# Kernel tuning notes

Measured on AMD Instinct MI355X. Metric: run time of the kernel, lower is better.

The kernel has to match this reference:

```python
import jax, jax.numpy as jnp
import numpy as np

B, T, N, D = 8, 64, 128, 128  # batch, timesteps, num_nodes, hidden_dim
LN_EPS = 1e-5
L2_EPS = 1e-12


def setup_inputs() -> dict:
    key = jax.random.key(0)
    ks = jax.random.split(key, 8)
    feat = jax.random.normal(ks[0], (B, T, N, D), dtype=jnp.float32)
    w = jax.random.uniform(ks[1], (D,), dtype=jnp.float32)  # learned adj gate (torch.rand init)
    s = 1.0 / np.sqrt(D)
    W1 = jax.random.uniform(ks[2], (D, D), dtype=jnp.float32, minval=-s, maxval=s)
    b1 = jax.random.uniform(ks[3], (D,), dtype=jnp.float32, minval=-s, maxval=s)
    W2 = jax.random.uniform(ks[4], (D, D), dtype=jnp.float32, minval=-s, maxval=s)
    b2 = jax.random.uniform(ks[5], (D,), dtype=jnp.float32, minval=-s, maxval=s)
    gamma = jnp.ones((D,), dtype=jnp.float32)
    beta = jnp.zeros((D,), dtype=jnp.float32)
    return {"feat": feat, "w": w, "W1": W1, "b1": b1, "W2": W2, "b2": b2,
            "gamma": gamma, "beta": beta}


def _windows(x):
    # x: (B, T, N, D) -> (B, T-2, 3*N, D): 3 consecutive timesteps flattened over nodes
    b, t, n, d = x.shape
    return jnp.stack([x[:, i:i + t - 2] for i in range(3)], axis=2).reshape(b, t - 2, 3 * n, d)


def reference(feat, w, W1, b1, W2, b2, gamma, beta):
    # gated + L2-normalized features for learned adjacency
    wf = feat * jax.nn.sigmoid(w)
    wf = wf / jnp.maximum(jnp.linalg.norm(wf, axis=-1, keepdims=True), L2_EPS)

    win = _windows(feat)   # (B, T-2, 3N, D)
    wwin = _windows(wf)    # (B, T-2, 3N, D)

    # learned adjacency: gram matrix per window, (B, T-2, 3N, 3N)
    adj = jnp.einsum('btmd,btnd->btmn', wwin, wwin)

    # symmetric normalization D^{-1/2} A D^{-1/2}; inf/nan (deg<=0) -> 0 as in torch
    deg = adj.sum(axis=-1, keepdims=True)
    dis = jnp.where(deg > 0, jax.lax.rsqrt(jnp.maximum(deg, 1e-38)), 0.0)
    nadj = dis * adj * jnp.swapaxes(dis, -1, -2)

    # message passing, keep last N rows (current timestep)
    agg = jnp.einsum('btmn,btnd->btmd', nadj, win)[:, :, -N:, :]

    # FFN (dropout is identity in eval): Linear -> ReLU -> Linear
    h = jax.nn.relu(agg @ W1 + b1) @ W2 + b2

    # residual with current-timestep features + LayerNorm
    s = feat[:, 2:] + h
    mu = s.mean(axis=-1, keepdims=True)
    var = ((s - mu) ** 2).mean(axis=-1, keepdims=True)
    return (s - mu) * jax.lax.rsqrt(var + LN_EPS) * gamma + beta
```

## Files before the change

### kernel.cpp

```cpp
#include <hip/hip_runtime.h>
#include <math.h>

#define BB    8
#define TDIM  64
#define NN    128
#define DD    128
#define TTOUT 62
#define W3    384

typedef __attribute__((ext_vector_type(8))) short bf16x8;
typedef __attribute__((ext_vector_type(4))) float f32x4;

__device__ __forceinline__ float sigf(float x){ return 1.0f/(1.0f+__expf(-x)); }
__device__ __forceinline__ unsigned short f2bf(float x){
  union{float f; unsigned u;} v; v.f=x;
  unsigned r = v.u + 0x7FFFu + ((v.u>>16)&1u);
  return (unsigned short)(r>>16);
}
__device__ __forceinline__ int swzA(int row, int col){ return row*128 + (col ^ ((row&7)<<3)); }
__device__ __forceinline__ int swzF(int row, int col){ return row*64  + (col ^ ((row&7)<<3)); }

__global__ __launch_bounds__(512) void k_pre(const float* __restrict__ feat,
    const float* __restrict__ w, const float* __restrict__ W1, const float* __restrict__ W2,
    float* __restrict__ rscale, float* __restrict__ ssum,
    unsigned short* __restrict__ W1T, unsigned short* __restrict__ W2T){
  __shared__ float sSig[DD];
  __shared__ float sRs[NN];
  __shared__ float sPart[4*DD];
  const int bid = blockIdx.x, tid = threadIdx.x;
  if(bid >= BB*TDIM){
    const float* W = (bid == BB*TDIM) ? W1 : W2;
    unsigned short* WT = (bid == BB*TDIM) ? W1T : W2T;
    for(int e=tid; e<DD*DD; e+=512){
      int k = e>>7, n = e&127;
      WT[n*DD + k] = f2bf(W[(size_t)k*DD + n]);
    }
    return;
  }
  const int bt = bid;
  if(tid < DD) sSig[tid] = sigf(w[tid]);
  __syncthreads();
  const int row = tid >> 2, q = tid & 3;
  const float* fp = feat + ((size_t)bt*NN + row)*DD + q*32;
  float ss = 0.f;
  #pragma unroll
  for(int i=0;i<8;i++){
    float4 v = *(const float4*)(fp + i*4);
    float g0 = v.x*sSig[q*32+i*4+0], g1 = v.y*sSig[q*32+i*4+1];
    float g2 = v.z*sSig[q*32+i*4+2], g3 = v.w*sSig[q*32+i*4+3];
    ss += g0*g0 + g1*g1 + g2*g2 + g3*g3;
  }
  ss += __shfl_xor(ss,1); ss += __shfl_xor(ss,2);
  float rs = 1.0f / fmaxf(sqrtf(ss), 1e-12f);
  if(q==0){ rscale[(size_t)bt*NN + row] = rs; sRs[row] = rs; }
  __syncthreads();
  const int d = tid & 127, rg = tid >> 7;
  const float* fc = feat + ((size_t)bt*NN + rg*32)*DD + d;
  float acc = 0.f;
  #pragma unroll 8
  for(int i=0;i<32;i++) acc += fc[(size_t)i*DD] * sRs[rg*32+i];
  sPart[rg*DD + d] = acc;
  __syncthreads();
  if(tid < DD)
    ssum[(size_t)bt*DD + tid] =
      (sPart[tid] + sPart[DD+tid] + sPart[2*DD+tid] + sPart[3*DD+tid]) * sSig[tid];
}

__global__ void k_dis(const float* __restrict__ feat, const float* __restrict__ w,
                      const float* __restrict__ rscale, const float* __restrict__ ssum,
                      float* __restrict__ dis){
  __shared__ float s3[DD];
  __shared__ float sg[DD];
  int bt2 = (blockIdx.x & 7)*62 + (blockIdx.x >> 3);
  int b = bt2 / TTOUT, tt = bt2 % TTOUT;
  int tid = threadIdx.x;
  if(tid < DD){
    int base = (b*TDIM + tt)*DD;
    s3[tid] = ssum[base+tid] + ssum[base+DD+tid] + ssum[base+2*DD+tid];
    sg[tid] = sigf(w[tid]);
  }
  __syncthreads();
  int gr = (b*TDIM + tt)*NN + tid;
  const float4* fr = (const float4*)(feat + (size_t)gr*DD);
  float deg = 0.f;
  #pragma unroll 8
  for(int q=0;q<DD/4;q++){
    float4 f = fr[q];
    deg += f.x*sg[q*4+0]*s3[q*4+0] + f.y*sg[q*4+1]*s3[q*4+1]
         + f.z*sg[q*4+2]*s3[q*4+2] + f.w*sg[q*4+3]*s3[q*4+3];
  }
  deg *= rscale[gr];
  dis[(size_t)bt2*W3 + tid] = (deg > 0.f) ? rsqrtf(fmaxf(deg, 1e-38f)) : 0.f;
}

__global__ __launch_bounds__(512,4) void k_main(
    const float* __restrict__ feat,
    const float* __restrict__ w,
    const float* __restrict__ rscale, const float* __restrict__ dis,
    const unsigned short* __restrict__ W1T, const float* __restrict__ b1,
    const unsigned short* __restrict__ W2T, const float* __restrict__ b2,
    const float* __restrict__ gamma, const float* __restrict__ beta,
    float* __restrict__ out)
{
  __shared__ __align__(16) unsigned short sm[36864];
  __shared__ float sSig[DD];
  unsigned short* sA  = sm;
  unsigned short* sG  = sm + 16384;
  unsigned short* sFt = sm + 20480;
  unsigned short* sP  = sm + 28672;
  unsigned short* sWt = sm + 16384;

  const int tid = threadIdx.x;
  const int bid = blockIdx.x;
  const int bt2 = (bid & 7)*62 + (bid >> 3);
  const int rowBase = (bt2/TTOUT)*TDIM*NN + (bt2%TTOUT)*NN;
  const float* disP = dis + (size_t)bt2*W3;

  const int lane = tid & 63, wid = tid >> 6;
  const int l15 = lane & 15, l4 = lane >> 4;
  const int m0 = wid * 16;

  if(tid < DD) sSig[tid] = sigf(w[tid]);
  __syncthreads();

  #pragma unroll
  for(int e0=0; e0<8; ++e0){
    int e = e0*512 + tid;
    int d = e & 127, r0 = (e>>7)*4;
    float sg = sSig[d];
    #pragma unroll
    for(int i=0;i<4;i++){
      int j = 256 + r0 + i, gr = rowBase + j;
      float f = feat[(size_t)gr*DD + d];
      float fac = rscale[gr]*disP[j];
      sA[swzA(r0+i, d)] = f2bf(f*sg*fac);
    }
  }

  f32x4 acc2[8];
  #pragma unroll
  for(int i=0;i<8;i++) acc2[i] = (f32x4){0.f,0.f,0.f,0.f};

  for(int c=0; c<12; ++c){
    const int n0 = c*32;
    __syncthreads();
    #pragma unroll
    for(int e0=0; e0<2; ++e0){
      int e = e0*512 + tid;
      int d = e & 127, r0 = (e>>7)*4;
      float sg = sSig[d];
      unsigned short fb[4];
      #pragma unroll
      for(int i=0;i<4;i++){
        int j = n0 + r0 + i, gr = rowBase + j;
        float f = feat[(size_t)gr*DD + d];
        float fac = rscale[gr]*disP[j];
        fb[i] = f2bf(f);
        sG[swzA(r0+i, d)] = f2bf(f*sg*fac);
      }
      unsigned int* fp = (unsigned int*)&sFt[swzF(d, r0)];
      fp[0] = (unsigned)fb[0] | ((unsigned)fb[1]<<16);
      fp[1] = (unsigned)fb[2] | ((unsigned)fb[3]<<16);
    }
    __syncthreads();

    f32x4 p0 = {0.f,0.f,0.f,0.f}, p1 = {0.f,0.f,0.f,0.f};
    #pragma unroll
    for(int ks=0; ks<4; ++ks){
      bf16x8 aA  = *(const bf16x8*)&sA[swzA(m0+l15, ks*32 + l4*8)];
      bf16x8 bg0 = *(const bf16x8*)&sG[swzA( 0+l15, ks*32 + l4*8)];
      bf16x8 bg1 = *(const bf16x8*)&sG[swzA(16+l15, ks*32 + l4*8)];
      p0 = __builtin_amdgcn_mfma_f32_16x16x32_bf16(aA, bg0, p0, 0,0,0);
      p1 = __builtin_amdgcn_mfma_f32_16x16x32_bf16(aA, bg1, p1, 0,0,0);
    }
    #pragma unroll
    for(int r=0;r<4;r++){
      sP[swzF(m0 + l4*4 + r,  0 + l15)] = f2bf(p0[r]);
      sP[swzF(m0 + l4*4 + r, 16 + l15)] = f2bf(p1[r]);
    }
    __syncthreads();

    bf16x8 aP = *(const bf16x8*)&sP[swzF(m0+l15, l4*8)];
    #pragma unroll
    for(int dt=0; dt<8; ++dt){
      bf16x8 bF = *(const bf16x8*)&sFt[swzF(dt*16+l15, l4*8)];
      acc2[dt] = __builtin_amdgcn_mfma_f32_16x16x32_bf16(aP, bF, acc2[dt], 0,0,0);
    }
  }

  unsigned short* ovl = sA;
  #pragma unroll
  for(int dt=0; dt<8; ++dt)
    #pragma unroll
    for(int r=0;r<4;r++)
      ovl[swzA(m0+l4*4+r, dt*16+l15)] = f2bf(acc2[dt][r]);

  f32x4 acch[8];
  #pragma unroll
  for(int dt=0; dt<8; ++dt){
    float bv = b1[dt*16+l15];
    acch[dt] = (f32x4){bv,bv,bv,bv};
  }
  for(int kh=0; kh<2; ++kh){
    __syncthreads();
    #pragma unroll
    for(int it=0; it<2; ++it){
      int e = it*512 + tid, n = e>>3, sg2 = e&7;
      uint4 v = *(const uint4*)(W1T + (size_t)n*DD + kh*64 + sg2*8);
      *(uint4*)&sWt[swzF(n, sg2*8)] = v;
    }
    __syncthreads();
    #pragma unroll
    for(int ks=0; ks<2; ++ks){
      bf16x8 aA = *(const bf16x8*)&ovl[swzA(m0+l15, kh*64 + ks*32 + l4*8)];
      #pragma unroll
      for(int dt=0; dt<8; ++dt){
        bf16x8 bW = *(const bf16x8*)&sWt[swzF(dt*16+l15, ks*32 + l4*8)];
        acch[dt] = __builtin_amdgcn_mfma_f32_16x16x32_bf16(aA, bW, acch[dt], 0,0,0);
      }
    }
  }
  __syncthreads();
  #pragma unroll
  for(int dt=0; dt<8; ++dt)
    #pragma unroll
    for(int r=0;r<4;r++)
      ovl[swzA(m0+l4*4+r, dt*16+l15)] = f2bf(fmaxf(acch[dt][r], 0.f));

  f32x4 acco[8];
  #pragma unroll
  for(int dt=0; dt<8; ++dt){
    float bv = b2[dt*16+l15];
    acco[dt] = (f32x4){bv,bv,bv,bv};
  }
  for(int kh=0; kh<2; ++kh){
    __syncthreads();
    #pragma unroll
    for(int it=0; it<2; ++it){
      int e = it*512 + tid, n = e>>3, sg2 = e&7;
      uint4 v = *(const uint4*)(W2T + (size_t)n*DD + kh*64 + sg2*8);
      *(uint4*)&sWt[swzF(n, sg2*8)] = v;
    }
    __syncthreads();
    #pragma unroll
    for(int ks=0; ks<2; ++ks){
      bf16x8 aA = *(const bf16x8*)&ovl[swzA(m0+l15, kh*64 + ks*32 + l4*8)];
      #pragma unroll
      for(int dt=0; dt<8; ++dt){
        bf16x8 bW = *(const bf16x8*)&sWt[swzF(dt*16+l15, ks*32 + l4*8)];
        acco[dt] = __builtin_amdgcn_mfma_f32_16x16x32_bf16(aA, bW, acco[dt], 0,0,0);
      }
    }
  }

  const float* fres = feat + (size_t)(rowBase + 256)*DD;
  #pragma unroll
  for(int r=0;r<4;r++){
    int m = m0 + l4*4 + r;
    float vals[8]; float s1 = 0.f, s2 = 0.f;
    #pragma unroll
    for(int dt=0; dt<8; ++dt){
      int d = dt*16 + l15;
      float v = acco[dt][r] + fres[(size_t)m*DD + d];
      vals[dt] = v; s1 += v; s2 += v*v;
    }
    #pragma unroll
    for(int k=1;k<16;k<<=1){ s1 += __shfl_xor(s1,k); s2 += __shfl_xor(s2,k); }
    float mu   = s1*(1.0f/DD);
    float rstd = rsqrtf(s2*(1.0f/DD) - mu*mu + 1e-5f);
    #pragma unroll
    for(int dt=0; dt<8; ++dt){
      int d = dt*16 + l15;
      out[((size_t)bt2*NN + m)*DD + d] = (vals[dt]-mu)*rstd*gamma[d] + beta[d];
    }
  }
}

extern "C" void kernel_launch(void* const* d_in, const int* in_sizes, int n_in,
                              void* d_out, int out_size, void* d_ws, size_t ws_size,
                              hipStream_t stream){
  const float* feat  = (const float*)d_in[0];
  const float* w     = (const float*)d_in[1];
  const float* W1    = (const float*)d_in[2];
  const float* b1    = (const float*)d_in[3];
  const float* W2    = (const float*)d_in[4];
  const float* b2    = (const float*)d_in[5];
  const float* gamma = (const float*)d_in[6];
  const float* beta  = (const float*)d_in[7];
  float* out = (float*)d_out;

  char* ws = (char*)d_ws;
  float* rscale = (float*)(ws + 0);
  float* ssum   = (float*)(ws + 262144);
  float* dis    = (float*)(ws + 524288);
  unsigned short* W1T = (unsigned short*)(ws + 1286144);
  unsigned short* W2T = (unsigned short*)(ws + 1318912);

  k_pre<<<BB*TDIM + 2, 512, 0, stream>>>(feat, w, W1, W2, rscale, ssum, W1T, W2T);
  k_dis<<<BB*TTOUT, W3, 0, stream>>>(feat, w, rscale, ssum, dis);
  k_main<<<BB*TTOUT, 512, 0, stream>>>(feat, w, rscale, dis, W1T, b1, W2T, b2,
                                       gamma, beta, out);
}
```

Baseline: 98.63 us.

## Keep A operand in registers, pad LDS layouts, shrink shared memory for occupancy

The current-timestep A-tile is now loaded directly from global memory into per-wave bf16 registers instead of being staged in LDS. The XOR swizzles are replaced with padded row strides, and the LDS buffers are re-aliased, cutting the shared footprint from about 72KB to about 52KB. Launch bounds go from 4 to 6 blocks per CU so that more blocks can be resident. The trade-off is extra register pressure under the tighter bound, possible spills, and padded layouts that may show different bank-conflict behaviour than the swizzle.

Result: slower. 152.6 us (+54.7%).

```diff
diff --git a/kernel.cpp b/kernel.cpp
--- a/kernel.cpp
+++ b/kernel.cpp
@@ -7,6 +7,9 @@
 #define DD    128
 #define TTOUT 62
 #define W3    384
+#define LG    136
+#define LP    40
+#define LW    68
 
 typedef __attribute__((ext_vector_type(8))) short bf16x8;
 typedef __attribute__((ext_vector_type(4))) float f32x4;
@@ -17,8 +20,6 @@
   unsigned r = v.u + 0x7FFFu + ((v.u>>16)&1u);
   return (unsigned short)(r>>16);
 }
-__device__ __forceinline__ int swzA(int row, int col){ return row*128 + (col ^ ((row&7)<<3)); }
-__device__ __forceinline__ int swzF(int row, int col){ return row*64  + (col ^ ((row&7)<<3)); }
 
 __global__ __launch_bounds__(512) void k_pre(const float* __restrict__ feat,
     const float* __restrict__ w, const float* __restrict__ W1, const float* __restrict__ W2,
@@ -93,7 +94,7 @@
   dis[(size_t)bt2*W3 + tid] = (deg > 0.f) ? rsqrtf(fmaxf(deg, 1e-38f)) : 0.f;
 }
 
-__global__ __launch_bounds__(512,4) void k_main(
+__global__ __launch_bounds__(512,6) void k_main(
     const float* __restrict__ feat,
     const float* __restrict__ w,
     const float* __restrict__ rscale, const float* __restrict__ dis,
@@ -102,13 +103,13 @@
     const float* __restrict__ gamma, const float* __restrict__ beta,
     float* __restrict__ out)
 {
-  __shared__ __align__(16) unsigned short sm[36864];
+  __shared__ __align__(16) unsigned short sm[26112];
   __shared__ float sSig[DD];
-  unsigned short* sA  = sm;
-  unsigned short* sG  = sm + 16384;
-  unsigned short* sFt = sm + 20480;
-  unsigned short* sP  = sm + 28672;
-  unsigned short* sWt = sm + 16384;
+  unsigned short* sG  = sm;
+  unsigned short* sFt = sm + 4352;
+  unsigned short* sP  = sm + 9472;
+  unsigned short* ovl = sm;
+  unsigned short* sWt = sm + 17408;
 
   const int tid = threadIdx.x;
   const int bid = blockIdx.x;
@@ -123,17 +124,22 @@
   if(tid < DD) sSig[tid] = sigf(w[tid]);
   __syncthreads();
 
-  #pragma unroll
-  for(int e0=0; e0<8; ++e0){
-    int e = e0*512 + tid;
-    int d = e & 127, r0 = (e>>7)*4;
-    float sg = sSig[d];
-    #pragma unroll
-    for(int i=0;i<4;i++){
-      int j = 256 + r0 + i, gr = rowBase + j;
-      float f = feat[(size_t)gr*DD + d];
-      float fac = rscale[gr]*disP[j];
-      sA[swzA(r0+i, d)] = f2bf(f*sg*fac);
+  bf16x8 aReg[4];
+  {
+    const int j = 256 + m0 + l15, gr = rowBase + j;
+    const float fac = rscale[gr]*disP[j];
+    const float* fr = feat + (size_t)gr*DD;
+    #pragma unroll
+    for(int ks=0; ks<4; ++ks){
+      float4 v0 = *(const float4*)(fr + ks*32 + l4*8);
+      float4 v1 = *(const float4*)(fr + ks*32 + l4*8 + 4);
+      const float* sg = sSig + ks*32 + l4*8;
+      unsigned short o[8];
+      o[0]=f2bf(v0.x*sg[0]*fac); o[1]=f2bf(v0.y*sg[1]*fac);
+      o[2]=f2bf(v0.z*sg[2]*fac); o[3]=f2bf(v0.w*sg[3]*fac);
+      o[4]=f2bf(v1.x*sg[4]*fac); o[5]=f2bf(v1.y*sg[5]*fac);
+      o[6]=f2bf(v1.z*sg[6]*fac); o[7]=f2bf(v1.w*sg[7]*fac);
+      aReg[ks] = *(bf16x8*)o;
     }
   }
 
@@ -156,9 +162,9 @@
         float f = feat[(size_t)gr*DD + d];
         float fac = rscale[gr]*disP[j];
         fb[i] = f2bf(f);
-        sG[swzA(r0+i, d)] = f2bf(f*sg*fac);
+        sG[(r0+i)*LG + d] = f2bf(f*sg*fac);
       }
-      unsigned int* fp = (unsigned int*)&sFt[swzF(d, r0)];
+      unsigned int* fp = (unsigned int*)&sFt[d*LP + r0];
       fp[0] = (unsigned)fb[0] | ((unsigned)fb[1]<<16);
       fp[1] = (unsigned)fb[2] | ((unsigned)fb[3]<<16);
     }
@@ -167,33 +173,33 @@
     f32x4 p0 = {0.f,0.f,0.f,0.f}, p1 = {0.f,0.f,0.f,0.f};
     #pragma unroll
     for(int ks=0; ks<4; ++ks){
-      bf16x8 aA  = *(const bf16x8*)&sA[swzA(m0+l15, ks*32 + l4*8)];
-      bf16x8 bg0 = *(const bf16x8*)&sG[swzA( 0+l15, ks*32 + l4*8)];
-      bf16x8 bg1 = *(const bf16x8*)&sG[swzA(16+l15, ks*32 + l4*8)];
-      p0 = __builtin_amdgcn_mfma_f32_16x16x32_bf16(aA, bg0, p0, 0,0,0);
-      p1 = __builtin_amdgcn_mfma_f32_16x16x32_bf16(aA, bg1, p1, 0,0,0);
+      bf16x8 bg0 = *(const bf16x8*)&sG[( 0+l15)*LG + ks*32 + l4*8];
+      bf16x8 bg1 = *(const bf16x8*)&sG[(16+l15)*LG + ks*32 + l4*8];
+      p0 = __builtin_amdgcn_mfma_f32_16x16x32_bf16(aReg[ks], bg0, p0, 0,0,0);
+      p1 = __builtin_amdgcn_mfma_f32_16x16x32_bf16(aReg[ks], bg1, p1, 0,0,0);
     }
     #pragma unroll
     for(int r=0;r<4;r++){
-      sP[swzF(m0 + l4*4 + r,  0 + l15)] = f2bf(p0[r]);
-      sP[swzF(m0 + l4*4 + r, 16 + l15)] = f2bf(p1[r]);
-    }
-    __syncthreads();
-
-    bf16x8 aP = *(const bf16x8*)&sP[swzF(m0+l15, l4*8)];
+      sP[(m0 + l4*4 + r)*LP +  0 + l15] = f2bf(p0[r]);
+      sP[(m0 + l4*4 + r)*LP + 16 + l15] = f2bf(p1[r]);
+    }
+    __syncthreads();
+
+    bf16x8 aP = *(const bf16x8*)&sP[(m0+l15)*LP + l4*8];
     #pragma unroll
     for(int dt=0; dt<8; ++dt){
-      bf16x8 bF = *(const bf16x8*)&sFt[swzF(dt*16+l15, l4*8)];
+      bf16x8 bF = *(const bf16x8*)&sFt[(dt*16+l15)*LP + l4*8];
       acc2[dt] = __builtin_amdgcn_mfma_f32_16x16x32_bf16(aP, bF, acc2[dt], 0,0,0);
     }
   }
 
-  unsigned short* ovl = sA;
+  __syncthreads();
+
   #pragma unroll
   for(int dt=0; dt<8; ++dt)
     #pragma unroll
     for(int r=0;r<4;r++)
-      ovl[swzA(m0+l4*4+r, dt*16+l15)] = f2bf(acc2[dt][r]);
+      ovl[(m0+l4*4+r)*LG + dt*16+l15] = f2bf(acc2[dt][r]);
 
   f32x4 acch[8];
   #pragma unroll
@@ -207,15 +213,15 @@
     for(int it=0; it<2; ++it){
       int e = it*512 + tid, n = e>>3, sg2 = e&7;
       uint4 v = *(const uint4*)(W1T + (size_t)n*DD + kh*64 + sg2*8);
-      *(uint4*)&sWt[swzF(n, sg2*8)] = v;
+      *(uint4*)&sWt[n*LW + sg2*8] = v;
     }
     __syncthreads();
     #pragma unroll
     for(int ks=0; ks<2; ++ks){
-      bf16x8 aA = *(const bf16x8*)&ovl[swzA(m0+l15, kh*64 + ks*32 + l4*8)];
+      bf16x8 aA = *(const bf16x8*)&ovl[(m0+l15)*LG + kh*64 + ks*32 + l4*8];
       #pragma unroll
       for(int dt=0; dt<8; ++dt){
-        bf16x8 bW = *(const bf16x8*)&sWt[swzF(dt*16+l15, ks*32 + l4*8)];
+        bf16x8 bW = *(const bf16x8*)&sWt[(dt*16+l15)*LW + ks*32 + l4*8];
         acch[dt] = __builtin_amdgcn_mfma_f32_16x16x32_bf16(aA, bW, acch[dt], 0,0,0);
       }
     }
@@ -225,7 +231,7 @@
   for(int dt=0; dt<8; ++dt)
     #pragma unroll
     for(int r=0;r<4;r++)
-      ovl[swzA(m0+l4*4+r, dt*16+l15)] = f2bf(fmaxf(acch[dt][r], 0.f));
+      ovl[(m0+l4*4+r)*LG + dt*16+l15] = f2bf(fmaxf(acch[dt][r], 0.f));
 
   f32x4 acco[8];
   #pragma unroll
@@ -239,15 +245,15 @@
     for(int it=0; it<2; ++it){
       int e = it*512 + tid, n = e>>3, sg2 = e&7;
       uint4 v = *(const uint4*)(W2T + (size_t)n*DD + kh*64 + sg2*8);
-      *(uint4*)&sWt[swzF(n, sg2*8)] = v;
+      *(uint4*)&sWt[n*LW + sg2*8] = v;
     }
     __syncthreads();
     #pragma unroll
     for(int ks=0; ks<2; ++ks){
-      bf16x8 aA = *(const bf16x8*)&ovl[swzA(m0+l15, kh*64 + ks*32 + l4*8)];
+      bf16x8 aA = *(const bf16x8*)&ovl[(m0+l15)*LG + kh*64 + ks*32 + l4*8];
       #pragma unroll
       for(int dt=0; dt<8; ++dt){
-        bf16x8 bW = *(const bf16x8*)&sWt[swzF(dt*16+l15, ks*32 + l4*8)];
+        bf16x8 bW = *(const bf16x8*)&sWt[(dt*16+l15)*LW + ks*32 + l4*8];
         acco[dt] = __builtin_amdgcn_mfma_f32_16x16x32_bf16(aA, bW, acco[dt], 0,0,0);
       }
     }
```
